# Performance work log

Measured on AMD Instinct MI355X. Metric: run time of the kernel, lower is better.

## Reference

```python
import jax, jax.numpy as jnp
import numpy as np
import math

B, S, D, H = 2, 4096, 768, 12
HD = D // H            # 64
BLK = 32               # MRA block size (hard-coded in the module)
NBR = S // BLK         # 128 blocks per row
NUM_BLOCK = 1024       # selected score blocks per (batch*head)
APPROX_MODE = "full"
FIRST_N = 0            # initial_prior_first_n_blocks
DIAG_N = 3             # initial_prior_diagonal_n_blocks
MB = B * H


def setup_inputs() -> dict:
    key = jax.random.key(0)
    ks = jax.random.split(key, 4)
    scale = 0.02
    return {
        "X": jax.random.normal(ks[0], (B, S, D), jnp.float32),
        "mask": jnp.ones((B, S), jnp.float32),
        "Wq": scale * jax.random.normal(ks[1], (D, D), jnp.float32),
        "bq": jnp.zeros((D,), jnp.float32),
        "Wk": scale * jax.random.normal(ks[2], (D, D), jnp.float32),
        "bk": jnp.zeros((D,), jnp.float32),
        "Wv": scale * jax.random.normal(ks[3], (D, D), jnp.float32),
        "bv": jnp.zeros((D,), jnp.float32),
    }


def _mra2_attention(Q, K, V, mask):
    # Q, K, V: [MB, S, HD]; mask: [MB, S] (float 0/1)
    inv_sqrt_d = 1.0 / math.sqrt(HD)
    Q = Q * mask[:, :, None]
    K = K * mask[:, :, None]
    V = V * mask[:, :, None]

    # ---- low-resolution (block-mean) logits ----
    token_count = mask.reshape(MB, NBR, BLK).sum(-1)                 # [MB, NBR]
    denom = token_count[:, :, None] + 1e-6
    Qh = Q.reshape(MB, NBR, BLK, HD).sum(2) / denom                  # [MB, NBR, HD]
    Kh = K.reshape(MB, NBR, BLK, HD).sum(2) / denom
    Vh = V.reshape(MB, NBR, BLK, HD).sum(2) / denom

    low_logit = jnp.einsum('bnd,bmd->bnm', Qh, Kh) * inv_sqrt_d      # [MB, NBR, NBR]
    row_max = low_logit.max(-1, keepdims=True)                        # [MB, NBR, 1] (before empty-pair masking)
    pair_empty = (token_count[:, None, :] * token_count[:, :, None]) < 0.5
    low_logit = low_logit - 1e4 * pair_empty.astype(low_logit.dtype)

    # ---- top-k block selection (no grad) ----
    prior = jax.lax.stop_gradient(low_logit - row_max)
    if DIAG_N > 0:
        off = DIAG_N // 2
        i = jnp.arange(NBR)
        band = (jnp.abs(i[:, None] - i[None, :]) <= off).astype(prior.dtype)
        prior = prior + band[None] * 5e3
    if FIRST_N > 0:
        prior = prior.at[:, :FIRST_N, :].add(5e3)
        prior = prior.at[:, :, :FIRST_N].add(5e3)
    top_vals, indices = jax.lax.top_k(prior.reshape(MB, -1), NUM_BLOCK)  # row-major flat idx = q_blk*NBR + k_blk
    threshold = top_vals.min(-1)
    selected_mask = (prior >= threshold[:, None, None]).astype(jnp.float32)  # 1 for selected low-res blocks

    rblk = indices // NBR   # query block index, [MB, NUM_BLOCK]
    cblk = indices % NBR    # key block index
    bidx = jnp.arange(MB)[:, None]

    Qb = Q.reshape(MB, NBR, BLK, HD)
    Kb = K.reshape(MB, NBR, BLK, HD)
    Vb = V.reshape(MB, NBR, BLK, HD)
    kmask = mask.reshape(MB, NBR, BLK)[bidx, cblk]                   # [MB, NB, 32k]

    Qg = Qb[bidx, rblk]                                              # [MB, NB, 32, HD]
    Kg = Kb[bidx, cblk]
    Vg = Vb[bidx, cblk]

    # ---- high-resolution sparse block logits ----
    logit = jnp.einsum('bnqd,bnkd->bnqk', Qg, Kg) * inv_sqrt_d       # [MB, NB, 32q, 32k]

    seg = (jnp.arange(MB)[:, None] * NBR + rblk).reshape(-1)         # segment id per block -> query row block
    blk_qmax = logit.max(-1).reshape(MB * NUM_BLOCK, BLK)            # per-query-token max within block
    max_rows = jax.ops.segment_max(blk_qmax, seg, num_segments=MB * NBR)
    max_rows = jnp.maximum(max_rows, -1e6).reshape(MB, NBR, BLK)     # guard rows w/o selected blocks
    max_vals = max_rows.reshape(MB, S)                               # per-token sparse row max
    max_scatter = max_rows[bidx, rblk]                               # [MB, NB, 32q]

    logit = logit - max_scatter[:, :, :, None]
    logit = logit - 1e4 * (1.0 - kmask[:, :, None, :])
    attn = jnp.exp(logit)

    blk_out = jnp.einsum('bnqk,bnkd->bnqd', attn, Vg)                # [MB, NB, 32, HD]
    high_out = jax.ops.segment_sum(
        blk_out.reshape(MB * NUM_BLOCK, BLK, HD), seg, num_segments=MB * NBR
    ).reshape(MB, S, HD)
    high_norm = jax.ops.segment_sum(
        attn.sum(-1).reshape(MB * NUM_BLOCK, BLK), seg, num_segments=MB * NBR
    ).reshape(MB, S)

    if APPROX_MODE == "full":
        # low-res attention over NON-selected blocks, weighted by token counts
        low_attn = jnp.exp(low_logit - row_max - 1e4 * selected_mask) * token_count[:, None, :]
        low_out = jnp.einsum('bnm,bmd->bnd', low_attn, Vh)           # [MB, NBR, HD]
        low_out = jnp.repeat(low_out[:, :, None, :], BLK, axis=2).reshape(MB, S, HD)
        low_norm = jnp.repeat(low_attn.sum(-1)[:, :, None], BLK, axis=2).reshape(MB, S)

        log_corr = jnp.repeat(row_max, BLK, axis=2).reshape(MB, S) - max_vals
        log_corr = log_corr * mask
        low_corr = jnp.exp(jnp.minimum(log_corr, 0.0))
        high_corr = jnp.exp(-jnp.maximum(log_corr, 0.0))

        out = (high_out * high_corr[:, :, None] + low_out * low_corr[:, :, None]) / (
            (high_norm * high_corr + low_norm * low_corr + 1e-6)[:, :, None]
        )
    else:  # "sparse"
        out = high_out / (high_norm[:, :, None] + 1e-6)
    return out


def reference(X, mask, Wq, bq, Wk, bk, Wv, bv):
    def proj(W, b):
        y = jnp.einsum('bsd,ed->bse', X, W) + b                       # nn.Linear: x @ W.T + b
        return y.reshape(B, S, H, HD).transpose(0, 2, 1, 3).reshape(MB, S, HD)

    Q, K, V = proj(Wq, bq), proj(Wk, bk), proj(Wv, bv)
    m = jnp.broadcast_to(mask[:, None, :], (B, H, S)).reshape(MB, S)
    out = _mra2_attention(Q, K, V, m)
    return out.reshape(B, H, S, HD).transpose(0, 2, 1, 3).reshape(B, S, D)
```

## Files before the change

### kernel.cpp

```cpp
#include <hip/hip_runtime.h>

typedef __bf16 bf16;
typedef float f32x4 __attribute__((ext_vector_type(4)));
typedef bf16 bf16x8 __attribute__((ext_vector_type(8)));
typedef bf16 bf16x4 __attribute__((ext_vector_type(4)));
typedef unsigned int uint;
typedef unsigned short ushort;


__device__ __forceinline__ void llds16(const bf16* g, bf16* l) {
    __builtin_amdgcn_global_load_lds((const __attribute__((address_space(1))) uint*)g,
                                     (__attribute__((address_space(3))) uint*)l, 16, 0, 0);
}

__device__ __forceinline__ uint sortable(float f) {
    uint u = __float_as_uint(f);
    return u ^ (uint)(((int)u >> 31) | 0x80000000);
}

__global__ __launch_bounds__(256)
void k_prep(const float* __restrict__ X, const float* __restrict__ mask,
            bf16* __restrict__ Xb, float* __restrict__ Xh, float* __restrict__ tc) {
    const int row = blockIdx.x;
    const int b = row >> 7, nbr = row & 127;
    const int g = blockIdx.y;
    const int t = threadIdx.x;
    const int c = t & 63;
    const int tq = t >> 6;
    const int c4 = g * 64 + c;
    const size_t base = (size_t)(b * 4096 + nbr * 32) * 768;
    const float4* xp = (const float4*)(X + base) + c4;
    bf16x4* xbp = (bf16x4*)(Xb + base) + c4;
    const float* mp = mask + b * 4096 + nbr * 32;
    __shared__ float4 red[4][64];
    __shared__ float tcr[4];
    float4 s = {0.f, 0.f, 0.f, 0.f};
    float tcs = 0.f;
#pragma unroll
    for (int j = 0; j < 8; ++j) {
        const int tok = tq * 8 + j;
        float4 v = xp[(size_t)tok * 192];
        float m = mp[tok];
        s.x += v.x * m; s.y += v.y * m; s.z += v.z * m; s.w += v.w * m;
        tcs += m;
        bf16x4 o = {(bf16)v.x, (bf16)v.y, (bf16)v.z, (bf16)v.w};
        xbp[(size_t)tok * 192] = o;
    }
    red[tq][c] = s;
    if (c == 0) tcr[tq] = tcs;
    __syncthreads();
    if (tq == 0) {
        float4 a = red[0][c], b2 = red[1][c], c2 = red[2][c], d2 = red[3][c];
        float4 o = {a.x + b2.x + c2.x + d2.x, a.y + b2.y + c2.y + d2.y,
                    a.z + b2.z + c2.z + d2.z, a.w + b2.w + c2.w + d2.w};
        ((float4*)(Xh + (size_t)row * 768))[c4] = o;
        if (c == 0 && g == 0) tc[row] = tcr[0] + tcr[1] + tcr[2] + tcr[3];
    }
}

__global__ void k_convW(const float* __restrict__ Wq, const float* __restrict__ Wk,
                        const float* __restrict__ Wv, bf16* __restrict__ Wb) {
    int i = blockIdx.x * 256 + threadIdx.x;
    if (i >= 442368) return;
    int n = (i << 2) / 768;
    int k = (i << 2) % 768;
    const float* W = n < 768 ? Wq : (n < 1536 ? Wk : Wv);
    int nn = n - (n < 768 ? 0 : (n < 1536 ? 768 : 1536));
    float4 f = *(const float4*)(W + (size_t)nn * 768 + k);
    bf16x4 o = {(bf16)f.x, (bf16)f.y, (bf16)f.z, (bf16)f.w};
    ((bf16x4*)Wb)[i] = o;
}

__global__ __launch_bounds__(256, 4)
void k_gemm_qkv(const bf16* __restrict__ Xb, const bf16* __restrict__ Wb,
                const float* __restrict__ bq, const float* __restrict__ bk,
                const float* __restrict__ bv, const float* __restrict__ mask,
                bf16* __restrict__ Qb, bf16* __restrict__ Kb, bf16* __restrict__ Vt) {
    __shared__ bf16 smem[17408];
    bf16* As = smem;
    bf16* Bs = smem + 8192;
    const int tid = threadIdx.x;
    const int wave = tid >> 6, lane = tid & 63;
    const int quad = lane >> 4, l16 = lane & 15;
    const int wr = wave >> 1, wc = wave & 1;
    const int m0 = blockIdx.x * 128, n0 = blockIdx.y * 128;
    const int srow = lane >> 3;
    const int sgcol = (((lane & 7) ^ (srow & 7)) << 3);

    f32x4 acc[4][4] = {};

    for (int k0 = 0; k0 < 768; k0 += 64) {
        __syncthreads();
#pragma unroll
        for (int it = 0; it < 4; ++it) {
            int R = wave * 32 + it * 8;
            llds16(Xb + (size_t)(m0 + R + srow) * 768 + k0 + sgcol, &As[R * 64]);
            llds16(Wb + (size_t)(n0 + R + srow) * 768 + k0 + sgcol, &Bs[R * 64]);
        }
        __syncthreads();
#pragma unroll
        for (int ks = 0; ks < 2; ++ks) {
            const int pg = ((ks * 4 + quad) ^ (l16 & 7)) << 3;
            bf16x8 a[4], b[4];
#pragma unroll
            for (int i = 0; i < 4; ++i)
                a[i] = *(const bf16x8*)&As[(wr * 64 + i * 16 + l16) * 64 + pg];
#pragma unroll
            for (int i = 0; i < 4; ++i)
                b[i] = *(const bf16x8*)&Bs[(wc * 64 + i * 16 + l16) * 64 + pg];
#pragma unroll
            for (int i = 0; i < 4; ++i)
#pragma unroll
                for (int j = 0; j < 4; ++j)
                    acc[i][j] = __builtin_amdgcn_mfma_f32_16x16x32_bf16(a[i], b[j], acc[i][j], 0, 0, 0);
        }
    }

    const int which = n0 / 768;
    const float* bias = which == 0 ? bq : (which == 1 ? bk : bv);

    __syncthreads();
#pragma unroll
    for (int i = 0; i < 4; ++i) {
        const int rloc0 = wr * 64 + i * 16 + quad * 4;
#pragma unroll
        for (int j = 0; j < 4; ++j) {
            const int cloc = wc * 64 + j * 16 + l16;
            const int hcol = n0 - which * 768 + cloc;
            const float bv_ = bias[hcol];
#pragma unroll
            for (int r = 0; r < 4; ++r) {
                const int rloc = rloc0 + r;
                const int mm = m0 + rloc;
                const int bidx = mm >> 12, s = mm & 4095;
                const float y = (acc[i][j][r] + bv_) * mask[(bidx << 12) + s];
                if (which == 2) smem[cloc * 136 + rloc] = (bf16)y;
                else            smem[rloc * 136 + cloc] = (bf16)y;
            }
        }
    }
    __syncthreads();
    if (which < 2) {
        bf16* dst = which == 0 ? Qb : Kb;
#pragma unroll
        for (int it = 0; it < 8; ++it) {
            const int gidx = it * 256 + tid;
            const int sr = gidx >> 4, chunk = gidx & 15;
            const int mm = m0 + sr;
            const int bidx = mm >> 12, s = mm & 4095;
            const int hcol = n0 - which * 768 + chunk * 8;
            const int h = hcol >> 6, d0 = hcol & 63;
            bf16x8 v = *(const bf16x8*)&smem[sr * 136 + chunk * 8];
            *(bf16x8*)(dst + ((((size_t)(bidx * 12 + h)) << 12) + s) * 64 + d0) = v;
        }
    } else {
#pragma unroll
        for (int it = 0; it < 8; ++it) {
            const int gidx = it * 256 + tid;
            const int drow = gidx >> 4, chunk = gidx & 15;
            const int s0 = chunk * 8;
            const int mm = m0 + s0;
            const int bidx = mm >> 12, s = mm & 4095;
            const int hcol = n0 - 1536 + drow;
            const int h = hcol >> 6, dd = hcol & 63;
            bf16x8 v = *(const bf16x8*)&smem[drow * 136 + s0];
            *(bf16x8*)(Vt + ((((size_t)(bidx * 12 + h)) * 128 + (s >> 5)) * 64 + dd) * 32 + (s & 31)) = v;
        }
    }
}

__global__ __launch_bounds__(256)
void k_lowres_p(const float* __restrict__ Xh,
                const float* __restrict__ Wq, const float* __restrict__ Wk,
                const float* __restrict__ Wv, float* __restrict__ partial) {
    const int nb = blockIdx.x;
    const int rowbase = blockIdx.y * 128;
    const int bz = blockIdx.z;
    const int kb = bz * 112;
    const int klen = (bz == 6) ? 96 : 112;
    const int t = threadIdx.x;

    __shared__ float As[16 * 132];
    __shared__ float Bs[16 * 132];

    const int which = nb / 6;
    const float* Wsel = which == 0 ? Wq : (which == 1 ? Wk : Wv);
    const float* Wbase = Wsel + (size_t)((nb % 6) * 128) * 768;

    const int sr = t >> 2;
    const int skq = t & 3;
    const int tr = t >> 4, tc2 = t & 15;
    const int r0 = tr * 8, c0 = tc2 * 8;

    float acc[8][8] = {};
    float4 va[2], vb[2];
    const int stages = klen >> 4;

#pragma unroll
    for (int i = 0; i < 2; ++i) {
        va[i] = *(const float4*)(Xh + (size_t)(rowbase + sr + 64 * i) * 768 + kb + skq * 4);
        vb[i] = *(const float4*)(Wbase + (size_t)(sr + 64 * i) * 768 + kb + skq * 4);
    }

    for (int s = 0; s < stages; ++s) {
        __syncthreads();
#pragma unroll
        for (int i = 0; i < 2; ++i) {
            const int r = sr + 64 * i;
            As[(skq * 4 + 0) * 132 + r] = va[i].x;
            As[(skq * 4 + 1) * 132 + r] = va[i].y;
            As[(skq * 4 + 2) * 132 + r] = va[i].z;
            As[(skq * 4 + 3) * 132 + r] = va[i].w;
            Bs[(skq * 4 + 0) * 132 + r] = vb[i].x;
            Bs[(skq * 4 + 1) * 132 + r] = vb[i].y;
            Bs[(skq * 4 + 2) * 132 + r] = vb[i].z;
            Bs[(skq * 4 + 3) * 132 + r] = vb[i].w;
        }
        if (s + 1 < stages) {
            const int kc = kb + (s + 1) * 16;
#pragma unroll
            for (int i = 0; i < 2; ++i) {
                va[i] = *(const float4*)(Xh + (size_t)(rowbase + sr + 64 * i) * 768 + kc + skq * 4);
                vb[i] = *(const float4*)(Wbase + (size_t)(sr + 64 * i) * 768 + kc + skq * 4);
            }
        }
        __syncthreads();
#pragma unroll
        for (int k = 0; k < 16; ++k) {
            float4 a0 = *(const float4*)&As[k * 132 + r0];
            float4 a1 = *(const float4*)&As[k * 132 + r0 + 4];
            float4 b0 = *(const float4*)&Bs[k * 132 + c0];
            float4 b1 = *(const float4*)&Bs[k * 132 + c0 + 4];
            float av[8] = {a0.x, a0.y, a0.z, a0.w, a1.x, a1.y, a1.z, a1.w};
            float bv[8] = {b0.x, b0.y, b0.z, b0.w, b1.x, b1.y, b1.z, b1.w};
#pragma unroll
            for (int i = 0; i < 8; ++i)
#pragma unroll
                for (int j = 0; j < 8; ++j)
                    acc[i][j] += av[i] * bv[j];
        }
    }

    float* pp = partial + (size_t)bz * 589824 + (size_t)(rowbase + r0) * 2304 + nb * 128 + c0;
#pragma unroll
    for (int i = 0; i < 8; ++i) {
        float4 s0 = {acc[i][0], acc[i][1], acc[i][2], acc[i][3]};
        float4 s1 = {acc[i][4], acc[i][5], acc[i][6], acc[i][7]};
        *(float4*)(pp + (size_t)i * 2304) = s0;
        *(float4*)(pp + (size_t)i * 2304 + 4) = s1;
    }
}

__global__ __launch_bounds__(256)
void k_lowfin(const float* __restrict__ partial, const float* __restrict__ tc,
              const float* __restrict__ bq, const float* __restrict__ bk,
              const float* __restrict__ bv,
              float* __restrict__ Qh, float* __restrict__ Kh, float* __restrict__ Vh) {
    const int gx = blockIdx.x;
    const int row = blockIdx.y;
    const int t = threadIdx.x;
    const int gcol = gx * 256 + t;
    float s = 0.f;
#pragma unroll
    for (int ch = 0; ch < 7; ++ch)
        s += partial[(size_t)ch * 589824 + (size_t)row * 2304 + gcol];
    const int which = gx / 3;
    const int wcol = (gx % 3) * 256 + t;
    const float* bias = which == 0 ? bq : (which == 1 ? bk : bv);
    const float tcv = tc[row];
    const float val = (s + tcv * bias[wcol]) / (tcv + 1e-6f);
    const int b = row >> 7, nbr = row & 127;
    const int h = wcol >> 6, d = wcol & 63;
    float* dst = which == 0 ? Qh : (which == 1 ? Kh : Vh);
    dst[(((size_t)(b * 12 + h)) * 128 + nbr) * 64 + d] = val;
}

__global__ __launch_bounds__(256)
void k_lowlogit(const float* __restrict__ Qh, const float* __restrict__ Kh,
                float* __restrict__ prior, float* __restrict__ rowmax) {
    int mb = blockIdx.x, rc = blockIdx.y;
    int tid = threadIdx.x;
    __shared__ float Ksh[64 * 132];
    __shared__ float Qsh[16 * 64];
    for (int idx = tid; idx < 128 * 64; idx += 256) {
        int c = idx >> 6, k = idx & 63;
        Ksh[k * 132 + c] = Kh[((size_t)mb * 128 + c) * 64 + k];
    }
    for (int idx = tid; idx < 16 * 64; idx += 256) {
        int r = idx >> 6, k = idx & 63;
        Qsh[idx] = Qh[((size_t)mb * 128 + rc * 16 + r) * 64 + k];
    }
    __syncthreads();
    int rloc = tid >> 4, cg = tid & 15;
    float acc[8] = {};
    for (int k = 0; k < 64; ++k) {
        float qv = Qsh[rloc * 64 + k];
        const float* kr = &Ksh[k * 132 + cg * 8];
#pragma unroll
        for (int j = 0; j < 8; ++j) acc[j] += qv * kr[j];
    }
    float pm = -3.4e38f;
#pragma unroll
    for (int j = 0; j < 8; ++j) { acc[j] *= 0.125f; pm = fmaxf(pm, acc[j]); }
#pragma unroll
    for (int d = 1; d < 16; d <<= 1) pm = fmaxf(pm, __shfl_xor(pm, d, 64));
    int r = rc * 16 + rloc;
    if (cg == 0) rowmax[mb * 128 + r] = pm;
    float* dst = prior + ((size_t)mb * 128 + r) * 128 + cg * 8;
#pragma unroll
    for (int j = 0; j < 8; ++j) dst[j] = acc[j] - pm;
}

__global__ __launch_bounds__(1024)
void k_select(const float* __restrict__ prior, unsigned char* __restrict__ selmask,
              unsigned short* __restrict__ lists, int* __restrict__ counts,
              ushort* __restrict__ qorder) {
    const int mb = blockIdx.x, tid = threadIdx.x;
    const int ln = tid & 63;
    __shared__ int lc[16 * 3];
    __shared__ int cnt[128];
    if (tid < 48) lc[tid] = 0;
    if (tid < 128) cnt[tid] = 0;

    const int r = tid >> 3;
    const int cbase = (tid & 7) << 4;
    uint key[16];
    const float4* P4 = (const float4*)(prior + (size_t)mb * 16384) + (tid << 2);
#pragma unroll
    for (int j4 = 0; j4 < 4; ++j4) {
        float4 v = P4[j4];
        float vv[4] = {v.x, v.y, v.z, v.w};
#pragma unroll
        for (int e = 0; e < 4; ++e) {
            int c = cbase + (j4 << 2) + e;
            float f = vv[e] + ((r - c <= 1 && c - r <= 1) ? 5e3f : 0.f);
            key[(j4 << 2) + e] = sortable(f);
        }
    }
    __syncthreads();

    uint pfx = 0u;
    int k = 1024;
#pragma unroll
    for (int lvl = 0; lvl < 16; ++lvl) {
        const int sh = 30 - 2 * lvl;
        const uint maskA = (lvl == 0) ? 0u : (0xFFFFFFFFu << (sh + 2));
        int c3 = 0, c2 = 0, c1 = 0;
#pragma unroll
        for (int j = 0; j < 16; ++j) {
            uint x = key[j];
            bool m = ((x ^ pfx) & maskA) == 0u;
            uint f = (x >> sh) & 3u;
            c3 += (m && f == 3u);
            c2 += (m && f == 2u);
            c1 += (m && f == 1u);
        }
#pragma unroll
        for (int d = 1; d < 64; d <<= 1) {
            c3 += __shfl_xor(c3, d, 64);
            c2 += __shfl_xor(c2, d, 64);
            c1 += __shfl_xor(c1, d, 64);
        }
        if (ln == 0) {
            atomicAdd(&lc[lvl * 3 + 0], c3);
            atomicAdd(&lc[lvl * 3 + 1], c2);
            atomicAdd(&lc[lvl * 3 + 2], c1);
        }
        __syncthreads();
        const int C3 = lc[lvl * 3 + 0], C2 = lc[lvl * 3 + 1], C1 = lc[lvl * 3 + 2];
        uint choose;
        if (C3 >= k)                { choose = 3u; }
        else if (C3 + C2 >= k)      { choose = 2u; k -= C3; }
        else if (C3 + C2 + C1 >= k) { choose = 1u; k -= C3 + C2; }
        else                        { choose = 0u; k -= C3 + C2 + C1; }
        pfx |= choose << sh;
    }
    const uint T = pfx;

    uint packed[4] = {0u, 0u, 0u, 0u};
#pragma unroll
    for (int j = 0; j < 16; ++j) {
        if (key[j] >= T) {
            packed[j >> 2] |= 1u << ((j & 3) << 3);
            int pos = atomicAdd(&cnt[r], 1);
            lists[((size_t)mb * 128 + r) * 128 + pos] = (unsigned short)(cbase + j);
        }
    }
    uint4 pk;
    pk.x = packed[0]; pk.y = packed[1]; pk.z = packed[2]; pk.w = packed[3];
    *(uint4*)(selmask + (size_t)mb * 16384 + (size_t)tid * 16) = pk;
    __syncthreads();
    if (tid < 128) {
        const int myc = cnt[tid];
        counts[mb * 128 + tid] = myc;
        int rank = 0;
        for (int j = 0; j < 128; ++j) {
            int cj = cnt[j];
            rank += (cj > myc) || (cj == myc && j < tid);
        }
        qorder[mb * 128 + rank] = (ushort)tid;
    }
}

__global__ __launch_bounds__(64)
void k_lowout(const float* __restrict__ prior, const unsigned char* __restrict__ selmask,
              const float* __restrict__ tc, const float* __restrict__ Vh,
              float* __restrict__ low_out, float* __restrict__ low_norm) {
    const int q = blockIdx.x & 127, mb = blockIdx.x >> 7;
    const int d = threadIdx.x;
    const float* pn = prior + ((size_t)mb * 128 + q) * 128;
    const uint4* smv = (const uint4*)(selmask + ((size_t)mb * 128 + q) * 128);
    uint sm32[32];
#pragma unroll
    for (int w = 0; w < 8; ++w) {
        uint4 u = smv[w];
        sm32[w * 4 + 0] = u.x; sm32[w * 4 + 1] = u.y;
        sm32[w * 4 + 2] = u.z; sm32[w * 4 + 3] = u.w;
    }
    const float* tcb = tc + (mb / 12) * 128;
    const float* Vb = Vh + (size_t)mb * 128 * 64;
    float acc = 0.f, nrm = 0.f;
#pragma unroll 4
    for (int c = 0; c < 128; ++c) {
        if (!((sm32[c >> 2] >> ((c & 3) << 3)) & 1u)) {
            float w = __expf(pn[c]) * tcb[c];
            acc += w * Vb[c * 64 + d];
            nrm += w;
        }
    }
    low_out[((size_t)mb * 128 + q) * 64 + d] = acc;
    if (d == 0) low_norm[mb * 128 + q] = nrm;
}

__global__ __launch_bounds__(64)
void k_high(const bf16* __restrict__ Qb, const bf16* __restrict__ Kb,
            const bf16* __restrict__ Vt, const int* __restrict__ counts,
            const unsigned short* __restrict__ lists, const ushort* __restrict__ qorder,
            const float* __restrict__ rowmax, const float* __restrict__ low_out,
            const float* __restrict__ low_norm, const float* __restrict__ mask,
            float* __restrict__ out) {
    const int mb = blockIdx.x >> 7;
    const int q = qorder[mb * 128 + (blockIdx.x & 127)];
    const int lane = threadIdx.x, quad = lane >> 4, l16 = lane & 15;
    __shared__ bf16 Pb[32 * 40];

    const bf16* Qbase = Qb + ((size_t)mb * 4096 + q * 32) * 64;
    bf16x8 qf[2][2];
#pragma unroll
    for (int mt = 0; mt < 2; ++mt)
#pragma unroll
        for (int ks = 0; ks < 2; ++ks)
            qf[mt][ks] = *(const bf16x8*)(Qbase + (mt * 16 + l16) * 64 + ks * 32 + quad * 8);

    bf16x8 ones;
#pragma unroll
    for (int j = 0; j < 8; ++j) ones[j] = (bf16)1.0f;

    float mxl[2][4];
    f32x4 o[2][4] = {};
    f32x4 lac[2] = {};
#pragma unroll
    for (int mt = 0; mt < 2; ++mt)
#pragma unroll
        for (int r = 0; r < 4; ++r) mxl[mt][r] = -3.4e38f;

    int cntv = counts[mb * 128 + q];
    if (cntv > 128) cntv = 128;
    if (cntv < 1) cntv = 1;
    const unsigned short* lst = lists + ((size_t)mb * 128 + q) * 128;

    const bf16* KB = Kb + (size_t)mb * 4096 * 64;
    const bf16* VB = Vt + (size_t)mb * 128 * 2048;

    int c0 = lst[0];
    bf16x8 kf_n[2][2], vf_n[4];
#pragma unroll
    for (int nt = 0; nt < 2; ++nt)
#pragma unroll
        for (int ks = 0; ks < 2; ++ks)
            kf_n[nt][ks] = *(const bf16x8*)(KB + ((size_t)c0 * 32 + nt * 16 + l16) * 64 + ks * 32 + quad * 8);
#pragma unroll
    for (int nd = 0; nd < 4; ++nd)
        vf_n[nd] = *(const bf16x8*)(VB + (size_t)c0 * 2048 + (nd * 16 + l16) * 32 + quad * 8);

    for (int i = 0; i < cntv; ++i) {
        bf16x8 kf[2][2], vf[4];
#pragma unroll
        for (int nt = 0; nt < 2; ++nt)
#pragma unroll
            for (int ks = 0; ks < 2; ++ks) kf[nt][ks] = kf_n[nt][ks];
#pragma unroll
        for (int nd = 0; nd < 4; ++nd) vf[nd] = vf_n[nd];

        if (i + 1 < cntv) {
            const int cn = lst[i + 1];
#pragma unroll
            for (int nt = 0; nt < 2; ++nt)
#pragma unroll
                for (int ks = 0; ks < 2; ++ks)
                    kf_n[nt][ks] = *(const bf16x8*)(KB + ((size_t)cn * 32 + nt * 16 + l16) * 64 + ks * 32 + quad * 8);
#pragma unroll
            for (int nd = 0; nd < 4; ++nd)
                vf_n[nd] = *(const bf16x8*)(VB + (size_t)cn * 2048 + (nd * 16 + l16) * 32 + quad * 8);
        }

        f32x4 sf[2][2] = {};
#pragma unroll
        for (int mt = 0; mt < 2; ++mt)
#pragma unroll
            for (int nt = 0; nt < 2; ++nt) {
                sf[mt][nt] = __builtin_amdgcn_mfma_f32_16x16x32_bf16(qf[mt][0], kf[nt][0], sf[mt][nt], 0, 0, 0);
                sf[mt][nt] = __builtin_amdgcn_mfma_f32_16x16x32_bf16(qf[mt][1], kf[nt][1], sf[mt][nt], 0, 0, 0);
            }

#pragma unroll
        for (int mt = 0; mt < 2; ++mt)
#pragma unroll
            for (int r = 0; r < 4; ++r) {
                mxl[mt][r] = fmaxf(mxl[mt][r], fmaxf(sf[mt][0][r], sf[mt][1][r]));
                Pb[(mt * 16 + quad * 4 + r) * 40 + 0 * 16 + l16] =
                    (bf16)exp2f(sf[mt][0][r] * 0.18033688011112042f);
                Pb[(mt * 16 + quad * 4 + r) * 40 + 1 * 16 + l16] =
                    (bf16)exp2f(sf[mt][1][r] * 0.18033688011112042f);
            }

        __syncthreads();
        bf16x8 pf[2];
#pragma unroll
        for (int mt = 0; mt < 2; ++mt)
            pf[mt] = *(const bf16x8*)&Pb[(mt * 16 + l16) * 40 + quad * 8];
#pragma unroll
        for (int mt = 0; mt < 2; ++mt) {
#pragma unroll
            for (int nd = 0; nd < 4; ++nd)
                o[mt][nd] = __builtin_amdgcn_mfma_f32_16x16x32_bf16(pf[mt], vf[nd], o[mt][nd], 0, 0, 0);
            lac[mt] = __builtin_amdgcn_mfma_f32_16x16x32_bf16(pf[mt], ones, lac[mt], 0, 0, 0);
        }
        __syncthreads();
    }

#pragma unroll
    for (int d = 1; d < 16; d <<= 1)
#pragma unroll
        for (int mt = 0; mt < 2; ++mt)
#pragma unroll
            for (int r = 0; r < 4; ++r)
                mxl[mt][r] = fmaxf(mxl[mt][r], __shfl_xor(mxl[mt][r], d, 64));

    const int b = mb / 12, h = mb - b * 12;
    const float rm = rowmax[mb * 128 + q];
    const float ln = low_norm[mb * 128 + q];
    const float* LO = low_out + ((size_t)mb * 128 + q) * 64;
#pragma unroll
    for (int mt = 0; mt < 2; ++mt)
#pragma unroll
        for (int r = 0; r < 4; ++r) {
            const int s = q * 32 + mt * 16 + quad * 4 + r;
            const float mv = fmaxf(mxl[mt][r] * 0.125f, -1e6f);
            const float hn = lac[mt][r];
            const float mk = mask[(b << 12) + s];
            const float lcr = (rm - mv) * mk;
            const float lcf = __expf(fminf(lcr, 0.f));
            const float hcf = __expf(-mv - fmaxf(lcr, 0.f));
            const float den = 1.0f / (hn * hcf + ln * lcf + 1e-6f);
            float* op = out + ((size_t)(b * 4096 + s)) * 768 + h * 64;
#pragma unroll
            for (int nd = 0; nd < 4; ++nd) {
                const int d = nd * 16 + l16;
                op[d] = (o[mt][nd][r] * hcf + LO[d] * lcf) * den;
            }
        }
}

extern "C" void kernel_launch(void* const* d_in, const int* in_sizes, int n_in,
                              void* d_out, int out_size, void* d_ws, size_t ws_size,
                              hipStream_t stream) {
    (void)in_sizes; (void)n_in; (void)out_size; (void)ws_size;
    const float* X    = (const float*)d_in[0];
    const float* mask = (const float*)d_in[1];
    const float* Wq   = (const float*)d_in[2];
    const float* bq   = (const float*)d_in[3];
    const float* Wk   = (const float*)d_in[4];
    const float* bk   = (const float*)d_in[5];
    const float* Wv   = (const float*)d_in[6];
    const float* bv   = (const float*)d_in[7];
    float* out = (float*)d_out;

    char* ws = (char*)d_ws;
    size_t off = 0;
    auto alloc = [&](size_t bytes) -> void* {
        off = (off + 255) & ~(size_t)255;
        void* p = ws + off;
        off += bytes;
        return p;
    };
    bf16* Xb  = (bf16*)alloc((size_t)8192 * 768 * 2);
    bf16* Wb  = (bf16*)alloc((size_t)2304 * 768 * 2);
    bf16* Qb  = (bf16*)alloc((size_t)24 * 4096 * 64 * 2);
    bf16* Kb  = (bf16*)alloc((size_t)24 * 4096 * 64 * 2);
    bf16* Vt  = (bf16*)alloc((size_t)24 * 4096 * 64 * 2);
    float* Xh = (float*)alloc((size_t)256 * 768 * 4);
    float* tc = (float*)alloc(256 * 4);
    float* Qh = (float*)alloc((size_t)24 * 128 * 64 * 4);
    float* Kh = (float*)alloc((size_t)24 * 128 * 64 * 4);
    float* Vh = (float*)alloc((size_t)24 * 128 * 64 * 4);
    float* prior = (float*)alloc((size_t)24 * 16384 * 4);
    float* rowmax = (float*)alloc(24 * 128 * 4);
    unsigned char* selmask = (unsigned char*)alloc((size_t)24 * 16384);
    unsigned short* lists = (unsigned short*)alloc((size_t)24 * 128 * 128 * 2);
    int* counts = (int*)alloc(24 * 128 * 4);
    ushort* qorder = (ushort*)alloc(24 * 128 * 2);
    float* low_out   = (float*)alloc((size_t)24 * 128 * 64 * 4);
    float* low_norm  = (float*)alloc(24 * 128 * 4);
    float* partial   = (float*)alloc((size_t)7 * 589824 * 4);

    k_prep<<<dim3(256, 3), 256, 0, stream>>>(X, mask, Xb, Xh, tc);
    k_convW<<<1728, 256, 0, stream>>>(Wq, Wk, Wv, Wb);
    k_gemm_qkv<<<dim3(64, 18), 256, 0, stream>>>(Xb, Wb, bq, bk, bv, mask, Qb, Kb, Vt);
    k_lowres_p<<<dim3(18, 2, 7), 256, 0, stream>>>(Xh, Wq, Wk, Wv, partial);
    k_lowfin<<<dim3(9, 256), 256, 0, stream>>>(partial, tc, bq, bk, bv, Qh, Kh, Vh);
    k_lowlogit<<<dim3(24, 8), 256, 0, stream>>>(Qh, Kh, prior, rowmax);
    k_select<<<24, 1024, 0, stream>>>(prior, selmask, lists, counts, qorder);
    k_lowout<<<3072, 64, 0, stream>>>(prior, selmask, tc, Vh, low_out, low_norm);
    k_high<<<3072, 64, 0, stream>>>(Qb, Kb, Vt, counts, lists, qorder, rowmax, low_out,
                                    low_norm, mask, out);
}
```

Measured before the change: 284.1 us.

## Split high-res block loop across four waves with LDS reduction in k_high

k_high now launches 256 threads per query block, and each wave handles every fourth selected key block with its own LDS P buffer. This removes the per-iteration block barriers. Partial outputs, row sums and row maxima are combined through shared memory before wave 0 writes the final result. The aim is to shorten each block's serial MFMA/load chain and raise occupancy, at the cost of extra LDS traffic and a reduction phase.

```diff
diff --git a/kernel.cpp b/kernel.cpp
--- a/kernel.cpp
+++ b/kernel.cpp
@@ -432,7 +432,7 @@
     if (d == 0) low_norm[mb * 128 + q] = nrm;
 }
 
-__global__ __launch_bounds__(64)
+__global__ __launch_bounds__(256)
 void k_high(const bf16* __restrict__ Qb, const bf16* __restrict__ Kb,
             const bf16* __restrict__ Vt, const int* __restrict__ counts,
             const unsigned short* __restrict__ lists, const ushort* __restrict__ qorder,
@@ -441,8 +441,14 @@
             float* __restrict__ out) {
     const int mb = blockIdx.x >> 7;
     const int q = qorder[mb * 128 + (blockIdx.x & 127)];
-    const int lane = threadIdx.x, quad = lane >> 4, l16 = lane & 15;
-    __shared__ bf16 Pb[32 * 40];
+    const int tid = threadIdx.x;
+    const int wid = tid >> 6;
+    const int lane = tid & 63, quad = lane >> 4, l16 = lane & 15;
+
+    __shared__ char un[17408] __attribute__((aligned(16)));
+    __shared__ float red_l[4][32];
+    __shared__ float red_m[4][32];
+    bf16* Pb = (bf16*)un + wid * 1280;
 
     const bf16* Qbase = Qb + ((size_t)mb * 4096 + q * 32) * 64;
     bf16x8 qf[2][2];
@@ -472,18 +478,21 @@
     const bf16* KB = Kb + (size_t)mb * 4096 * 64;
     const bf16* VB = Vt + (size_t)mb * 128 * 2048;
 
-    int c0 = lst[0];
+    int i = wid;
     bf16x8 kf_n[2][2], vf_n[4];
-#pragma unroll
-    for (int nt = 0; nt < 2; ++nt)
-#pragma unroll
-        for (int ks = 0; ks < 2; ++ks)
-            kf_n[nt][ks] = *(const bf16x8*)(KB + ((size_t)c0 * 32 + nt * 16 + l16) * 64 + ks * 32 + quad * 8);
-#pragma unroll
-    for (int nd = 0; nd < 4; ++nd)
-        vf_n[nd] = *(const bf16x8*)(VB + (size_t)c0 * 2048 + (nd * 16 + l16) * 32 + quad * 8);
-
-    for (int i = 0; i < cntv; ++i) {
+    if (i < cntv) {
+        const int c0 = lst[i];
+#pragma unroll
+        for (int nt = 0; nt < 2; ++nt)
+#pragma unroll
+            for (int ks = 0; ks < 2; ++ks)
+                kf_n[nt][ks] = *(const bf16x8*)(KB + ((size_t)c0 * 32 + nt * 16 + l16) * 64 + ks * 32 + quad * 8);
+#pragma unroll
+        for (int nd = 0; nd < 4; ++nd)
+            vf_n[nd] = *(const bf16x8*)(VB + (size_t)c0 * 2048 + (nd * 16 + l16) * 32 + quad * 8);
+    }
+
+    for (; i < cntv; i += 4) {
         bf16x8 kf[2][2], vf[4];
 #pragma unroll
         for (int nt = 0; nt < 2; ++nt)
@@ -492,8 +501,8 @@
 #pragma unroll
         for (int nd = 0; nd < 4; ++nd) vf[nd] = vf_n[nd];
 
-        if (i + 1 < cntv) {
-            const int cn = lst[i + 1];
+        if (i + 4 < cntv) {
+            const int cn = lst[i + 4];
 #pragma unroll
             for (int nt = 0; nt < 2; ++nt)
 #pragma unroll
@@ -524,7 +533,7 @@
                     (bf16)exp2f(sf[mt][1][r] * 0.18033688011112042f);
             }
 
-        __syncthreads();
+        asm volatile("s_waitcnt lgkmcnt(0)" ::: "memory");
         bf16x8 pf[2];
 #pragma unroll
         for (int mt = 0; mt < 2; ++mt)
@@ -536,7 +545,6 @@
                 o[mt][nd] = __builtin_amdgcn_mfma_f32_16x16x32_bf16(pf[mt], vf[nd], o[mt][nd], 0, 0, 0);
             lac[mt] = __builtin_amdgcn_mfma_f32_16x16x32_bf16(pf[mt], ones, lac[mt], 0, 0, 0);
         }
-        __syncthreads();
     }
 
 #pragma unroll
@@ -546,6 +554,64 @@
 #pragma unroll
             for (int r = 0; r < 4; ++r)
                 mxl[mt][r] = fmaxf(mxl[mt][r], __shfl_xor(mxl[mt][r], d, 64));
+
+    if (l16 == 0) {
+#pragma unroll
+        for (int mt = 0; mt < 2; ++mt)
+#pragma unroll
+            for (int r = 0; r < 4; ++r) {
+                const int row = mt * 16 + quad * 4 + r;
+                red_l[wid][row] = lac[mt][r];
+                red_m[wid][row] = mxl[mt][r];
+            }
+    }
+    __syncthreads();
+
+    float* red_o = (float*)un;
+    if (wid >= 2) {
+        float* ro = red_o + (wid - 2) * 2176;
+#pragma unroll
+        for (int mt = 0; mt < 2; ++mt)
+#pragma unroll
+            for (int nd = 0; nd < 4; ++nd)
+#pragma unroll
+                for (int r = 0; r < 4; ++r)
+                    ro[(mt * 16 + quad * 4 + r) * 68 + nd * 16 + l16] = o[mt][nd][r];
+    }
+    __syncthreads();
+    if (wid < 2) {
+        float* ro = red_o + wid * 2176;
+#pragma unroll
+        for (int mt = 0; mt < 2; ++mt)
+#pragma unroll
+            for (int nd = 0; nd < 4; ++nd)
+#pragma unroll
+                for (int r = 0; r < 4; ++r)
+                    o[mt][nd][r] += ro[(mt * 16 + quad * 4 + r) * 68 + nd * 16 + l16];
+    }
+    if (wid == 1) {
+        float* ro = red_o + 2176;
+#pragma unroll
+        for (int mt = 0; mt < 2; ++mt)
+#pragma unroll
+            for (int nd = 0; nd < 4; ++nd)
+#pragma unroll
+                for (int r = 0; r < 4; ++r)
+                    ro[(mt * 16 + quad * 4 + r) * 68 + nd * 16 + l16] = o[mt][nd][r];
+    }
+    __syncthreads();
+    if (wid != 0) return;
+
+    {
+        float* ro = red_o + 2176;
+#pragma unroll
+        for (int mt = 0; mt < 2; ++mt)
+#pragma unroll
+            for (int nd = 0; nd < 4; ++nd)
+#pragma unroll
+                for (int r = 0; r < 4; ++r)
+                    o[mt][nd][r] += ro[(mt * 16 + quad * 4 + r) * 68 + nd * 16 + l16];
+    }
 
     const int b = mb / 12, h = mb - b * 12;
     const float rm = rowmax[mb * 128 + q];
@@ -555,9 +621,12 @@
     for (int mt = 0; mt < 2; ++mt)
 #pragma unroll
         for (int r = 0; r < 4; ++r) {
-            const int s = q * 32 + mt * 16 + quad * 4 + r;
-            const float mv = fmaxf(mxl[mt][r] * 0.125f, -1e6f);
-            const float hn = lac[mt][r];
+            const int row = mt * 16 + quad * 4 + r;
+            const int s = q * 32 + row;
+            const float mm = fmaxf(fmaxf(red_m[0][row], red_m[1][row]),
+                                   fmaxf(red_m[2][row], red_m[3][row]));
+            const float hn = red_l[0][row] + red_l[1][row] + red_l[2][row] + red_l[3][row];
+            const float mv = fmaxf(mm * 0.125f, -1e6f);
             const float mk = mask[(b << 12) + s];
             const float lcr = (rm - mv) * mk;
             const float lcf = __expf(fminf(lcr, 0.f));
@@ -622,6 +691,6 @@
     k_lowlogit<<<dim3(24, 8), 256, 0, stream>>>(Qh, Kh, prior, rowmax);
     k_select<<<24, 1024, 0, stream>>>(prior, selmask, lists, counts, qorder);
     k_lowout<<<3072, 64, 0, stream>>>(prior, selmask, tc, Vh, low_out, low_norm);
-    k_high<<<3072, 64, 0, stream>>>(Qb, Kb, Vt, counts, lists, qorder, rowmax, low_out,
-                                    low_norm, mask, out);
-}
+    k_high<<<3072, 256, 0, stream>>>(Qb, Kb, Vt, counts, lists, qorder, rowmax, low_out,
+                                     low_norm, mask, out);
+}
```

New measurement: 284.0 us. No clear change (-0.0%).

## Process two key blocks per iteration in k_high with double-buffered P and prefetch

Applied to the files above, without the earlier changes.

The high-resolution attention loop now handles two selected key blocks per iteration, each with its own shared P tile. It reads block indices as packed 32-bit pairs made wave-uniform with readfirstlane, and prefetches the next pair's K and V separately so their latency overlaps the MFMAs. Since the block is a single wave, the two __syncthreads per block are replaced by an lgkmcnt wait, and exp2f becomes raw v_exp_f32. This raises register pressure, and skipping the barrier relies on single-wave LDS ordering between the P writes and later reads.

```diff
diff --git a/kernel.cpp b/kernel.cpp
--- a/kernel.cpp
+++ b/kernel.cpp
@@ -442,7 +442,8 @@
     const int mb = blockIdx.x >> 7;
     const int q = qorder[mb * 128 + (blockIdx.x & 127)];
     const int lane = threadIdx.x, quad = lane >> 4, l16 = lane & 15;
-    __shared__ bf16 Pb[32 * 40];
+    __shared__ bf16 Pa[32 * 40];
+    __shared__ bf16 Pbs[32 * 40];
 
     const bf16* Qbase = Qb + ((size_t)mb * 4096 + q * 32) * 64;
     bf16x8 qf[2][2];
@@ -467,76 +468,150 @@
     int cntv = counts[mb * 128 + q];
     if (cntv > 128) cntv = 128;
     if (cntv < 1) cntv = 1;
-    const unsigned short* lst = lists + ((size_t)mb * 128 + q) * 128;
+    const uint* lst32 = (const uint*)(lists + ((size_t)mb * 128 + q) * 128);
 
     const bf16* KB = Kb + (size_t)mb * 4096 * 64;
     const bf16* VB = Vt + (size_t)mb * 128 * 2048;
 
-    int c0 = lst[0];
-    bf16x8 kf_n[2][2], vf_n[4];
+    int koff[2][2], voff[4];
 #pragma unroll
     for (int nt = 0; nt < 2; ++nt)
 #pragma unroll
-        for (int ks = 0; ks < 2; ++ks)
-            kf_n[nt][ks] = *(const bf16x8*)(KB + ((size_t)c0 * 32 + nt * 16 + l16) * 64 + ks * 32 + quad * 8);
-#pragma unroll
-    for (int nd = 0; nd < 4; ++nd)
-        vf_n[nd] = *(const bf16x8*)(VB + (size_t)c0 * 2048 + (nd * 16 + l16) * 32 + quad * 8);
-
-    for (int i = 0; i < cntv; ++i) {
-        bf16x8 kf[2][2], vf[4];
+        for (int ks = 0; ks < 2; ++ks) koff[nt][ks] = (nt * 16 + l16) * 64 + ks * 32 + quad * 8;
+#pragma unroll
+    for (int nd = 0; nd < 4; ++nd) voff[nd] = (nd * 16 + l16) * 32 + quad * 8;
+
+    bf16x8 kA[2][2], vA[4], kB[2][2], vB[4];
+    {
+        const uint pr = lst32[0];
+        const int cA = __builtin_amdgcn_readfirstlane((int)(pr & 0xffffu));
+        const bf16* kp = KB + (size_t)cA * 2048;
+        const bf16* vp = VB + (size_t)cA * 2048;
 #pragma unroll
         for (int nt = 0; nt < 2; ++nt)
 #pragma unroll
-            for (int ks = 0; ks < 2; ++ks) kf[nt][ks] = kf_n[nt][ks];
-#pragma unroll
-        for (int nd = 0; nd < 4; ++nd) vf[nd] = vf_n[nd];
-
-        if (i + 1 < cntv) {
-            const int cn = lst[i + 1];
+            for (int ks = 0; ks < 2; ++ks) kA[nt][ks] = *(const bf16x8*)(kp + koff[nt][ks]);
+#pragma unroll
+        for (int nd = 0; nd < 4; ++nd) vA[nd] = *(const bf16x8*)(vp + voff[nd]);
+        if (cntv > 1) {
+            const int cB = __builtin_amdgcn_readfirstlane((int)(pr >> 16));
+            const bf16* kp2 = KB + (size_t)cB * 2048;
+            const bf16* vp2 = VB + (size_t)cB * 2048;
 #pragma unroll
             for (int nt = 0; nt < 2; ++nt)
 #pragma unroll
-                for (int ks = 0; ks < 2; ++ks)
-                    kf_n[nt][ks] = *(const bf16x8*)(KB + ((size_t)cn * 32 + nt * 16 + l16) * 64 + ks * 32 + quad * 8);
+                for (int ks = 0; ks < 2; ++ks) kB[nt][ks] = *(const bf16x8*)(kp2 + koff[nt][ks]);
+#pragma unroll
+            for (int nd = 0; nd < 4; ++nd) vB[nd] = *(const bf16x8*)(vp2 + voff[nd]);
+        }
+    }
+
+    for (int i = 0; i < cntv; i += 2) {
+        const bool hasB = (i + 1 < cntv);
+        const bool hasAn = (i + 2 < cntv);
+        const bool hasBn = (i + 3 < cntv);
+        int cAn = 0, cBn = 0;
+        if (hasAn) {
+            const uint prn = lst32[(i >> 1) + 1];
+            cAn = __builtin_amdgcn_readfirstlane((int)(prn & 0xffffu));
+            cBn = __builtin_amdgcn_readfirstlane((int)(prn >> 16));
+        }
+
+        {
+            f32x4 sf[2][2] = {};
+#pragma unroll
+            for (int mt = 0; mt < 2; ++mt)
+#pragma unroll
+                for (int nt = 0; nt < 2; ++nt) {
+                    sf[mt][nt] = __builtin_amdgcn_mfma_f32_16x16x32_bf16(qf[mt][0], kA[nt][0], sf[mt][nt], 0, 0, 0);
+                    sf[mt][nt] = __builtin_amdgcn_mfma_f32_16x16x32_bf16(qf[mt][1], kA[nt][1], sf[mt][nt], 0, 0, 0);
+                }
+#pragma unroll
+            for (int mt = 0; mt < 2; ++mt)
+#pragma unroll
+                for (int r = 0; r < 4; ++r) {
+                    mxl[mt][r] = fmaxf(mxl[mt][r], fmaxf(sf[mt][0][r], sf[mt][1][r]));
+                    float e0, e1;
+                    asm("v_exp_f32 %0, %1" : "=v"(e0) : "v"(sf[mt][0][r] * 0.18033688011112042f));
+                    asm("v_exp_f32 %0, %1" : "=v"(e1) : "v"(sf[mt][1][r] * 0.18033688011112042f));
+                    Pa[(mt * 16 + quad * 4 + r) * 40 + l16] = (bf16)e0;
+                    Pa[(mt * 16 + quad * 4 + r) * 40 + 16 + l16] = (bf16)e1;
+                }
+        }
+        if (hasB) {
+            f32x4 sf[2][2] = {};
+#pragma unroll
+            for (int mt = 0; mt < 2; ++mt)
+#pragma unroll
+                for (int nt = 0; nt < 2; ++nt) {
+                    sf[mt][nt] = __builtin_amdgcn_mfma_f32_16x16x32_bf16(qf[mt][0], kB[nt][0], sf[mt][nt], 0, 0, 0);
+                    sf[mt][nt] = __builtin_amdgcn_mfma_f32_16x16x32_bf16(qf[mt][1], kB[nt][1], sf[mt][nt], 0, 0, 0);
+                }
+#pragma unroll
+            for (int mt = 0; mt < 2; ++mt)
+#pragma unroll
+                for (int r = 0; r < 4; ++r) {
+                    mxl[mt][r] = fmaxf(mxl[mt][r], fmaxf(sf[mt][0][r], sf[mt][1][r]));
+                    float e0, e1;
+                    asm("v_exp_f32 %0, %1" : "=v"(e0) : "v"(sf[mt][0][r] * 0.18033688011112042f));
+                    asm("v_exp_f32 %0, %1" : "=v"(e1) : "v"(sf[mt][1][r] * 0.18033688011112042f));
+                    Pbs[(mt * 16 + quad * 4 + r) * 40 + l16] = (bf16)e0;
+                    Pbs[(mt * 16 + quad * 4 + r) * 40 + 16 + l16] = (bf16)e1;
+                }
+        }
+
+        if (hasAn) {
+            const bf16* kp = KB + (size_t)cAn * 2048;
+#pragma unroll
+            for (int nt = 0; nt < 2; ++nt)
+#pragma unroll
+                for (int ks = 0; ks < 2; ++ks) kA[nt][ks] = *(const bf16x8*)(kp + koff[nt][ks]);
+        }
+        if (hasBn) {
+            const bf16* kp = KB + (size_t)cBn * 2048;
+#pragma unroll
+            for (int nt = 0; nt < 2; ++nt)
+#pragma unroll
+                for (int ks = 0; ks < 2; ++ks) kB[nt][ks] = *(const bf16x8*)(kp + koff[nt][ks]);
+        }
+
+        asm volatile("s_waitcnt lgkmcnt(0)" ::: "memory");
+        bf16x8 pa[2], pb[2];
+#pragma unroll
+        for (int mt = 0; mt < 2; ++mt)
+            pa[mt] = *(const bf16x8*)&Pa[(mt * 16 + l16) * 40 + quad * 8];
+        if (hasB) {
+#pragma unroll
+            for (int mt = 0; mt < 2; ++mt)
+                pb[mt] = *(const bf16x8*)&Pbs[(mt * 16 + l16) * 40 + quad * 8];
+        }
+#pragma unroll
+        for (int mt = 0; mt < 2; ++mt) {
 #pragma unroll
             for (int nd = 0; nd < 4; ++nd)
-                vf_n[nd] = *(const bf16x8*)(VB + (size_t)cn * 2048 + (nd * 16 + l16) * 32 + quad * 8);
-        }
-
-        f32x4 sf[2][2] = {};
-#pragma unroll
-        for (int mt = 0; mt < 2; ++mt)
-#pragma unroll
-            for (int nt = 0; nt < 2; ++nt) {
-                sf[mt][nt] = __builtin_amdgcn_mfma_f32_16x16x32_bf16(qf[mt][0], kf[nt][0], sf[mt][nt], 0, 0, 0);
-                sf[mt][nt] = __builtin_amdgcn_mfma_f32_16x16x32_bf16(qf[mt][1], kf[nt][1], sf[mt][nt], 0, 0, 0);
+                o[mt][nd] = __builtin_amdgcn_mfma_f32_16x16x32_bf16(pa[mt], vA[nd], o[mt][nd], 0, 0, 0);
+            lac[mt] = __builtin_amdgcn_mfma_f32_16x16x32_bf16(pa[mt], ones, lac[mt], 0, 0, 0);
+        }
+        if (hasB) {
+#pragma unroll
+            for (int mt = 0; mt < 2; ++mt) {
+#pragma unroll
+                for (int nd = 0; nd < 4; ++nd)
+                    o[mt][nd] = __builtin_amdgcn_mfma_f32_16x16x32_bf16(pb[mt], vB[nd], o[mt][nd], 0, 0, 0);
+                lac[mt] = __builtin_amdgcn_mfma_f32_16x16x32_bf16(pb[mt], ones, lac[mt], 0, 0, 0);
             }
-
-#pragma unroll
-        for (int mt = 0; mt < 2; ++mt)
-#pragma unroll
-            for (int r = 0; r < 4; ++r) {
-                mxl[mt][r] = fmaxf(mxl[mt][r], fmaxf(sf[mt][0][r], sf[mt][1][r]));
-                Pb[(mt * 16 + quad * 4 + r) * 40 + 0 * 16 + l16] =
-                    (bf16)exp2f(sf[mt][0][r] * 0.18033688011112042f);
-                Pb[(mt * 16 + quad * 4 + r) * 40 + 1 * 16 + l16] =
-                    (bf16)exp2f(sf[mt][1][r] * 0.18033688011112042f);
-            }
-
-        __syncthreads();
-        bf16x8 pf[2];
-#pragma unroll
-        for (int mt = 0; mt < 2; ++mt)
-            pf[mt] = *(const bf16x8*)&Pb[(mt * 16 + l16) * 40 + quad * 8];
-#pragma unroll
-        for (int mt = 0; mt < 2; ++mt) {
-#pragma unroll
-            for (int nd = 0; nd < 4; ++nd)
-                o[mt][nd] = __builtin_amdgcn_mfma_f32_16x16x32_bf16(pf[mt], vf[nd], o[mt][nd], 0, 0, 0);
-            lac[mt] = __builtin_amdgcn_mfma_f32_16x16x32_bf16(pf[mt], ones, lac[mt], 0, 0, 0);
-        }
-        __syncthreads();
+        }
+
+        if (hasAn) {
+            const bf16* vp = VB + (size_t)cAn * 2048;
+#pragma unroll
+            for (int nd = 0; nd < 4; ++nd) vA[nd] = *(const bf16x8*)(vp + voff[nd]);
+        }
+        if (hasBn) {
+            const bf16* vp = VB + (size_t)cBn * 2048;
+#pragma unroll
+            for (int nd = 0; nd < 4; ++nd) vB[nd] = *(const bf16x8*)(vp + voff[nd]);
+        }
     }
 
 #pragma unroll
```

New measurement: 269.8 us. -5.0%, faster.
